# Optimization experiments

Measured on AMD Instinct MI355X. Metric: run time of the kernel, lower is better.

The kernel has to match this reference:

```python
import jax, jax.numpy as jnp
import numpy as np

B, NS, F_IN, H, DEG = 128, 200, 200, 128, 64
N = B * NS
E = B * NS * DEG


def leaky_relu(v):
    return jnp.where(v > 0, v, 0.01 * v)


def gcn_conv(x, W, b, src, dst, w_pos):
    # PyG GCNConv with add_self_loops=True (self-loop weight 1) and
    # symmetric deg^{-1/2} normalization; aggregation flows src -> dst.
    n = x.shape[0]
    deg = jax.ops.segment_sum(w_pos, dst, num_segments=n) + 1.0  # +1 from self-loop
    dinv = jnp.where(deg > 0, deg ** -0.5, 0.0)
    norm = dinv[src] * w_pos * dinv[dst]          # [E]
    xw = x @ W                                     # [N,H]
    msg = norm[:, None] * xw[src]                  # [E,H]
    out = jax.ops.segment_sum(msg, dst, num_segments=n)
    out = out + (dinv * dinv)[:, None] * xw        # self-loop: norm = deg^{-1}
    return out + b


def setup_inputs() -> dict:
    key = jax.random.key(0)
    ks = jax.random.split(key, 14)
    # edges: each node gets DEG incoming edges from random nodes in SAME graph
    src_local = jax.random.randint(ks[0], (B, NS * DEG), 0, NS)
    dst_local = jnp.tile(jnp.repeat(jnp.arange(NS), DEG)[None, :], (B, 1))
    offsets = (jnp.arange(B) * NS)[:, None]
    src = (src_local + offsets).reshape(-1).astype(jnp.int32)
    dst = (dst_local + offsets).reshape(-1).astype(jnp.int32)
    edge_index = jnp.stack([src, dst])             # [2,E]
    edge_weight = jax.random.normal(ks[1], (E,), dtype=jnp.float32)  # mixed sign
    x = jax.random.normal(ks[2], (N, F_IN), dtype=jnp.float32)
    s = 0.05
    p = {
        'W0': jax.random.normal(ks[3], (F_IN, H)) * s, 'b0': jnp.zeros((H,)),
        'W1': jax.random.normal(ks[4], (H, H)) * s,    'b1': jnp.zeros((H,)),
        'W2': jax.random.normal(ks[5], (H, H)) * s,    'b2': jnp.zeros((H,)),
        'lincomb_W': jax.random.normal(ks[6], (NS * H, H)) * 0.01,
        'lincomb_b': jnp.zeros((H,)),
        'fc1_W': jax.random.normal(ks[7], (H, H // 2)) * s, 'fc1_b': jnp.zeros((H // 2,)),
        'fc2_W': jax.random.normal(ks[8], (H // 2, H // 4)) * s, 'fc2_b': jnp.zeros((H // 4,)),
        'fc3_W': jax.random.normal(ks[9], (H // 4, 1)) * s, 'fc3_b': jnp.zeros((1,)),
    }
    return {'x': x, 'edge_index': edge_index, 'edge_weight': edge_weight, **p}


def reference(x, edge_index, edge_weight,
              W0, b0, W1, b1, W2, b2,
              lincomb_W, lincomb_b,
              fc1_W, fc1_b, fc2_W, fc2_b, fc3_W, fc3_b):
    src, dst = edge_index[0], edge_index[1]
    # convert_edge_positive: dropping non-positive edges == zeroing their weight
    w_pos = jnp.where(edge_weight > 0, edge_weight, 0.0)
    h = gcn_conv(x, W0, b0, src, dst, w_pos)
    h = leaky_relu(h)
    h = gcn_conv(h, W1, b1, src, dst, w_pos)
    h = leaky_relu(h)
    h = gcn_conv(h, W2, b2, src, dst, w_pos)  # no activation on last layer
    # per-graph flatten + lincomb
    g = h.reshape(B, NS * H) @ lincomb_W + lincomb_b   # [B,H]
    g = leaky_relu(g @ fc1_W + fc1_b)
    g = leaky_relu(g @ fc2_W + fc2_b)
    out = g @ fc3_W + fc3_b                            # [B,1]
    return out
```

## Files before the change

### kernel.cpp

```cpp
#include <hip/hip_runtime.h>

#define B_GRAPHS 128
#define NSN      200
#define F_INPUT  200
#define HDIM     128
#define DEG      64
#define N_NODES  (B_GRAPHS * NSN)
#define E_EDGES  (N_NODES * DEG)

__global__ __launch_bounds__(256) void k_dinv(const float* __restrict__ ew,
                                              float* __restrict__ dinv) {
  const int node = blockIdx.x * 4 + (threadIdx.x >> 6);
  const int lane = threadIdx.x & 63;
  float w = ew[(size_t)node * DEG + lane];
  w = w > 0.f ? w : 0.f;
  #pragma unroll
  for (int off = 32; off > 0; off >>= 1) w += __shfl_down(w, off);
  if (lane == 0) dinv[node] = rsqrtf(w + 1.0f);
}

__global__ __launch_bounds__(256) void k_norm(const int* __restrict__ src,
                                              const int* __restrict__ dst,
                                              const float* __restrict__ ew,
                                              const float* __restrict__ dinv,
                                              float* __restrict__ nrm) {
  const int e = blockIdx.x * 256 + threadIdx.x;
  float w = ew[e];
  w = w > 0.f ? w : 0.f;
  nrm[e] = dinv[src[e]] * w * dinv[dst[e]];
}

template <int F>
__global__ __launch_bounds__(256) void k_gemm(const float* __restrict__ X,
                                              const float* __restrict__ W,
                                              float* __restrict__ out) {
  __shared__ float Xs[64][8];
  __shared__ float Ws[8][128];
  const int t  = threadIdx.x;
  const int tx = t & 31;
  const int ty = t >> 5;
  const size_t row0 = (size_t)blockIdx.x * 64;
  float acc[8][4] = {};
  for (int k0 = 0; k0 < F; k0 += 8) {
    {
      const int i = t * 2;
      const int r = i >> 3, kk = i & 7;
      const float2 v = *reinterpret_cast<const float2*>(X + (row0 + r) * F + (k0 + kk));
      Xs[r][kk] = v.x; Xs[r][kk + 1] = v.y;
    }
    {
      const int j = t * 4;
      const int kk = j >> 7, col = j & 127;
      const float4 v = *reinterpret_cast<const float4*>(W + (size_t)(k0 + kk) * HDIM + col);
      *reinterpret_cast<float4*>(&Ws[kk][col]) = v;
    }
    __syncthreads();
    float xr[8][8];
    #pragma unroll
    for (int ii = 0; ii < 8; ++ii) {
      const float4 a = *reinterpret_cast<const float4*>(&Xs[ty * 8 + ii][0]);
      const float4 b = *reinterpret_cast<const float4*>(&Xs[ty * 8 + ii][4]);
      xr[ii][0] = a.x; xr[ii][1] = a.y; xr[ii][2] = a.z; xr[ii][3] = a.w;
      xr[ii][4] = b.x; xr[ii][5] = b.y; xr[ii][6] = b.z; xr[ii][7] = b.w;
    }
    #pragma unroll
    for (int kk = 0; kk < 8; ++kk) {
      const float4 wq = *reinterpret_cast<const float4*>(&Ws[kk][tx * 4]);
      const float wv[4] = {wq.x, wq.y, wq.z, wq.w};
      #pragma unroll
      for (int ii = 0; ii < 8; ++ii)
        #pragma unroll
        for (int jj = 0; jj < 4; ++jj)
          acc[ii][jj] = fmaf(xr[ii][kk], wv[jj], acc[ii][jj]);
    }
    __syncthreads();
  }
  #pragma unroll
  for (int ii = 0; ii < 8; ++ii) {
    const float4 v = {acc[ii][0], acc[ii][1], acc[ii][2], acc[ii][3]};
    *reinterpret_cast<float4*>(out + (row0 + ty * 8 + ii) * HDIM + tx * 4) = v;
  }
}

__global__ __launch_bounds__(256) void k_agg(const float* __restrict__ xw,
                                             const int* __restrict__ src,
                                             const float* __restrict__ nrm,
                                             const float* __restrict__ dinv,
                                             const float* __restrict__ bias,
                                             float* __restrict__ out,
                                             const int leaky) {
  const int node = blockIdx.x * 4 + (threadIdx.x >> 6);
  const int lane = threadIdx.x & 63;
  const int s_k  = src[(size_t)node * DEG + lane];
  const float n_k = nrm[(size_t)node * DEG + lane];
  float ax = 0.f, ay = 0.f;
  #pragma unroll 8
  for (int k = 0; k < DEG; ++k) {
    const int   s  = __shfl(s_k, k);
    const float nv = __shfl(n_k, k);
    const float2 v = *reinterpret_cast<const float2*>(xw + (size_t)s * HDIM + lane * 2);
    ax = fmaf(nv, v.x, ax);
    ay = fmaf(nv, v.y, ay);
  }
  const float di = dinv[node];
  const float sc = di * di;
  const float2 xv = *reinterpret_cast<const float2*>(xw + (size_t)node * HDIM + lane * 2);
  ax = fmaf(sc, xv.x, ax);
  ay = fmaf(sc, xv.y, ay);
  const float2 bv = *reinterpret_cast<const float2*>(bias + lane * 2);
  ax += bv.x; ay += bv.y;
  if (leaky) {
    ax = ax > 0.f ? ax : 0.01f * ax;
    ay = ay > 0.f ? ay : 0.01f * ay;
  }
  *reinterpret_cast<float2*>(out + (size_t)node * HDIM + lane * 2) = make_float2(ax, ay);
}

__global__ __launch_bounds__(256) void k_lincomb(const float* __restrict__ h,
                                                 const float* __restrict__ Wl,
                                                 float* __restrict__ P) {
  const int i = blockIdx.x;
  __shared__ float As[128][8];
  __shared__ float Bs[8][128];
  const int t   = threadIdx.x;
  const int txx = t & 15;
  const int ty  = t >> 4;
  float acc[8][8] = {};
  for (int k0 = 0; k0 < HDIM; k0 += 8) {
    {
      const int idx = t * 4;
      const int r = idx >> 3, kk = idx & 7;
      const float4 v = *reinterpret_cast<const float4*>(
          h + ((size_t)r * NSN + i) * HDIM + k0 + kk);
      As[r][kk] = v.x; As[r][kk + 1] = v.y; As[r][kk + 2] = v.z; As[r][kk + 3] = v.w;
    }
    {
      const int idx = t * 4;
      const int kk = idx >> 7, col = idx & 127;
      const float4 v = *reinterpret_cast<const float4*>(
          Wl + ((size_t)i * HDIM + k0 + kk) * HDIM + col);
      *reinterpret_cast<float4*>(&Bs[kk][col]) = v;
    }
    __syncthreads();
    #pragma unroll
    for (int kk = 0; kk < 8; ++kk) {
      float av[8], bv[8];
      #pragma unroll
      for (int ii = 0; ii < 8; ++ii) av[ii] = As[ty * 8 + ii][kk];
      #pragma unroll
      for (int jj = 0; jj < 8; ++jj) bv[jj] = Bs[kk][txx + jj * 16];
      #pragma unroll
      for (int ii = 0; ii < 8; ++ii)
        #pragma unroll
        for (int jj = 0; jj < 8; ++jj)
          acc[ii][jj] = fmaf(av[ii], bv[jj], acc[ii][jj]);
    }
    __syncthreads();
  }
  #pragma unroll
  for (int ii = 0; ii < 8; ++ii)
    #pragma unroll
    for (int jj = 0; jj < 8; ++jj)
      P[((size_t)i * B_GRAPHS + ty * 8 + ii) * HDIM + txx + jj * 16] = acc[ii][jj];
}

__global__ __launch_bounds__(256) void k_reduce(const float* __restrict__ P,
                                                const float* __restrict__ bl,
                                                float* __restrict__ g) {
  const int idx = blockIdx.x * 256 + threadIdx.x;
  float s0 = 0.f, s1 = 0.f, s2 = 0.f, s3 = 0.f;
  #pragma unroll 4
  for (int i = 0; i < NSN; i += 4) {
    s0 += P[(size_t)(i + 0) * (B_GRAPHS * HDIM) + idx];
    s1 += P[(size_t)(i + 1) * (B_GRAPHS * HDIM) + idx];
    s2 += P[(size_t)(i + 2) * (B_GRAPHS * HDIM) + idx];
    s3 += P[(size_t)(i + 3) * (B_GRAPHS * HDIM) + idx];
  }
  g[idx] = (s0 + s1) + (s2 + s3) + bl[idx & 127];
}

__global__ __launch_bounds__(64) void k_fc(const float* __restrict__ g,
                                           const float* __restrict__ f1W,
                                           const float* __restrict__ f1b,
                                           const float* __restrict__ f2W,
                                           const float* __restrict__ f2b,
                                           const float* __restrict__ f3W,
                                           const float* __restrict__ f3b,
                                           float* __restrict__ out) {
  const int b = blockIdx.x, t = threadIdx.x;
  __shared__ float gb[128];
  __shared__ float a1[64];
  __shared__ float a2[32];
  gb[t]      = g[(size_t)b * HDIM + t];
  gb[t + 64] = g[(size_t)b * HDIM + t + 64];
  __syncthreads();
  float acc = f1b[t];
  #pragma unroll 8
  for (int c = 0; c < 128; ++c) acc = fmaf(gb[c], f1W[c * 64 + t], acc);
  a1[t] = acc > 0.f ? acc : 0.01f * acc;
  __syncthreads();
  if (t < 32) {
    float a = f2b[t];
    #pragma unroll 8
    for (int c = 0; c < 64; ++c) a = fmaf(a1[c], f2W[c * 32 + t], a);
    a2[t] = a > 0.f ? a : 0.01f * a;
  }
  __syncthreads();
  if (t == 0) {
    float a = f3b[0];
    #pragma unroll
    for (int c = 0; c < 32; ++c) a = fmaf(a2[c], f3W[c], a);
    out[b] = a;
  }
}

extern "C" void kernel_launch(void* const* d_in, const int* in_sizes, int n_in,
                              void* d_out, int out_size, void* d_ws, size_t ws_size,
                              hipStream_t stream) {
  const float* x   = (const float*)d_in[0];
  const int*   ei  = (const int*)  d_in[1];
  const float* ew  = (const float*)d_in[2];
  const float* W0  = (const float*)d_in[3];
  const float* b0  = (const float*)d_in[4];
  const float* W1  = (const float*)d_in[5];
  const float* b1  = (const float*)d_in[6];
  const float* W2  = (const float*)d_in[7];
  const float* b2  = (const float*)d_in[8];
  const float* Wl  = (const float*)d_in[9];
  const float* bl  = (const float*)d_in[10];
  const float* f1W = (const float*)d_in[11];
  const float* f1b = (const float*)d_in[12];
  const float* f2W = (const float*)d_in[13];
  const float* f2b = (const float*)d_in[14];
  const float* f3W = (const float*)d_in[15];
  const float* f3b = (const float*)d_in[16];
  float* out = (float*)d_out;

  const int* src = ei;
  const int* dst = ei + E_EDGES;

  float* dinv = (float*)d_ws;
  float* nrm  = dinv + 32768;
  float* xw   = nrm + E_EDGES;
  float* hA   = xw + (size_t)N_NODES * HDIM;
  float* hB   = hA + (size_t)N_NODES * HDIM;
  float* P    = hB;
  float* g    = hB + (size_t)N_NODES * HDIM;

  k_dinv<<<N_NODES / 4, 256, 0, stream>>>(ew, dinv);
  k_norm<<<E_EDGES / 256, 256, 0, stream>>>(src, dst, ew, dinv, nrm);

  k_gemm<F_INPUT><<<N_NODES / 64, 256, 0, stream>>>(x, W0, xw);
  k_agg<<<N_NODES / 4, 256, 0, stream>>>(xw, src, nrm, dinv, b0, hA, 1);
  k_gemm<HDIM><<<N_NODES / 64, 256, 0, stream>>>(hA, W1, xw);
  k_agg<<<N_NODES / 4, 256, 0, stream>>>(xw, src, nrm, dinv, b1, hB, 1);
  k_gemm<HDIM><<<N_NODES / 64, 256, 0, stream>>>(hB, W2, xw);
  k_agg<<<N_NODES / 4, 256, 0, stream>>>(xw, src, nrm, dinv, b2, hA, 0);

  k_lincomb<<<NSN, 256, 0, stream>>>(hA, Wl, P);
  k_reduce<<<(B_GRAPHS * HDIM) / 256, 256, 0, stream>>>(P, bl, g);
  k_fc<<<B_GRAPHS, 64, 0, stream>>>(g, f1W, f1b, f2W, f2b, f3W, f3b, out);
}
```

Before: 383.5 us.

## Stage per-graph node features in LDS for GCN aggregation gathers

The aggregation kernel now gives each graph to two 512-thread blocks. Each block copies the whole graph's 200x128 transformed feature tile into shared memory and gathers neighbour rows from LDS instead of from global memory. This relies on all edges staying inside one graph and is meant to replace scattered global/L2 gathers with LDS reads. In exchange each block uses 100KB of LDS, which limits occupancy to about one block per CU, and only 256 blocks are launched. Each tile is also loaded twice, once per half.

```diff
diff --git a/kernel.cpp b/kernel.cpp
--- a/kernel.cpp
+++ b/kernel.cpp
@@ -82,38 +82,54 @@
   }
 }
 
-__global__ __launch_bounds__(256) void k_agg(const float* __restrict__ xw,
+__global__ __launch_bounds__(512) void k_agg(const float* __restrict__ xw,
                                              const int* __restrict__ src,
                                              const float* __restrict__ nrm,
                                              const float* __restrict__ dinv,
                                              const float* __restrict__ bias,
                                              float* __restrict__ out,
                                              const int leaky) {
-  const int node = blockIdx.x * 4 + (threadIdx.x >> 6);
-  const int lane = threadIdx.x & 63;
-  const int s_k  = src[(size_t)node * DEG + lane];
-  const float n_k = nrm[(size_t)node * DEG + lane];
-  float ax = 0.f, ay = 0.f;
-  #pragma unroll 8
-  for (int k = 0; k < DEG; ++k) {
-    const int   s  = __shfl(s_k, k);
-    const float nv = __shfl(n_k, k);
-    const float2 v = *reinterpret_cast<const float2*>(xw + (size_t)s * HDIM + lane * 2);
-    ax = fmaf(nv, v.x, ax);
-    ay = fmaf(nv, v.y, ay);
-  }
-  const float di = dinv[node];
-  const float sc = di * di;
-  const float2 xv = *reinterpret_cast<const float2*>(xw + (size_t)node * HDIM + lane * 2);
-  ax = fmaf(sc, xv.x, ax);
-  ay = fmaf(sc, xv.y, ay);
+  __shared__ float xs[NSN * HDIM];
+  const int g    = blockIdx.x >> 1;
+  const int half = blockIdx.x & 1;
+  const int t    = threadIdx.x;
+  const int w    = t >> 6;
+  const int lane = t & 63;
+
+  {
+    const float4* s4 = reinterpret_cast<const float4*>(xw + (size_t)g * NSN * HDIM);
+    float4* d4 = reinterpret_cast<float4*>(xs);
+    for (int i = t; i < NSN * HDIM / 4; i += 512) d4[i] = s4[i];
+  }
+  __syncthreads();
+
   const float2 bv = *reinterpret_cast<const float2*>(bias + lane * 2);
-  ax += bv.x; ay += bv.y;
-  if (leaky) {
-    ax = ax > 0.f ? ax : 0.01f * ax;
-    ay = ay > 0.f ? ay : 0.01f * ay;
-  }
-  *reinterpret_cast<float2*>(out + (size_t)node * HDIM + lane * 2) = make_float2(ax, ay);
+  const float2* xs2 = reinterpret_cast<const float2*>(xs);
+
+  for (int nloc = half * 100 + w; nloc < half * 100 + 100; nloc += 8) {
+    const int ng = g * NSN + nloc;
+    const int   s_k = src[(size_t)ng * DEG + lane] - g * NSN;
+    const float n_k = nrm[(size_t)ng * DEG + lane];
+    float ax = 0.f, ay = 0.f;
+    #pragma unroll
+    for (int k = 0; k < DEG; ++k) {
+      const int   s  = __shfl(s_k, k);
+      const float nv = __shfl(n_k, k);
+      const float2 v = xs2[s * (HDIM / 2) + lane];
+      ax = fmaf(nv, v.x, ax);
+      ay = fmaf(nv, v.y, ay);
+    }
+    const float di = dinv[ng];
+    const float sc = di * di;
+    const float2 xv = xs2[nloc * (HDIM / 2) + lane];
+    ax = fmaf(sc, xv.x, ax) + bv.x;
+    ay = fmaf(sc, xv.y, ay) + bv.y;
+    if (leaky) {
+      ax = ax > 0.f ? ax : 0.01f * ax;
+      ay = ay > 0.f ? ay : 0.01f * ay;
+    }
+    *reinterpret_cast<float2*>(out + (size_t)ng * HDIM + lane * 2) = make_float2(ax, ay);
+  }
 }
 
 __global__ __launch_bounds__(256) void k_lincomb(const float* __restrict__ h,
@@ -251,11 +267,11 @@
   k_norm<<<E_EDGES / 256, 256, 0, stream>>>(src, dst, ew, dinv, nrm);
 
   k_gemm<F_INPUT><<<N_NODES / 64, 256, 0, stream>>>(x, W0, xw);
-  k_agg<<<N_NODES / 4, 256, 0, stream>>>(xw, src, nrm, dinv, b0, hA, 1);
+  k_agg<<<B_GRAPHS * 2, 512, 0, stream>>>(xw, src, nrm, dinv, b0, hA, 1);
   k_gemm<HDIM><<<N_NODES / 64, 256, 0, stream>>>(hA, W1, xw);
-  k_agg<<<N_NODES / 4, 256, 0, stream>>>(xw, src, nrm, dinv, b1, hB, 1);
+  k_agg<<<B_GRAPHS * 2, 512, 0, stream>>>(xw, src, nrm, dinv, b1, hB, 1);
   k_gemm<HDIM><<<N_NODES / 64, 256, 0, stream>>>(hB, W2, xw);
-  k_agg<<<N_NODES / 4, 256, 0, stream>>>(xw, src, nrm, dinv, b2, hA, 0);
+  k_agg<<<B_GRAPHS * 2, 512, 0, stream>>>(xw, src, nrm, dinv, b2, hA, 0);
 
   k_lincomb<<<NSN, 256, 0, stream>>>(hA, Wl, P);
   k_reduce<<<(B_GRAPHS * HDIM) / 256, 256, 0, stream>>>(P, bl, g);
```

New measurement: 374.0 us. -2.5%, faster.
